# Optimization experiments

Measured on AMD Instinct MI355X. Metric: run time of the kernel, lower is better.

The kernel has to match this reference:

```python
import jax, jax.numpy as jnp
import numpy as np

TEMPERATURE = 0.1


def setup_inputs() -> dict:
    key = jax.random.key(0)
    k1, k2 = jax.random.split(key)
    B, D = 4096, 128
    z_i = jax.random.normal(k1, (B, D), dtype=jnp.float32)
    z_j = jax.random.normal(k2, (B, D), dtype=jnp.float32)
    return {"z_i": z_i, "z_j": z_j}


def reference(z_i, z_j):
    B = z_i.shape[0]
    n = 2 * B
    z = jnp.concatenate([z_i, z_j], axis=0)            # [2B, D]
    sim = jnp.matmul(z, z.T) / TEMPERATURE             # [2B, 2B]
    # positives: diag(sim, +B) and diag(sim, -B)
    pos = jnp.concatenate([jnp.diagonal(sim, B), jnp.diagonal(sim, -B)])[:, None]  # [2B, 1]
    # negatives: sim with diagonal removed, row-wise -> [2B, 2B-1]
    # strided trick equivalent to sim[~eye].reshape(n, n-1)
    neg = sim.ravel()[:-1].reshape(n - 1, n + 1)[:, 1:].reshape(n, n - 1)
    logits = jnp.concatenate([pos, neg], axis=1)       # [2B, 2B]
    # cross-entropy with labels all zero (positive in column 0)
    loss = jnp.mean(jax.nn.logsumexp(logits, axis=1) - logits[:, 0])
    return loss
```

## Files before the change

### kernel.cpp

```cpp
#include <hip/hip_runtime.h>
#include <stdint.h>

#define N_TOT  8192
#define BHALF  4096
#define DDIM   128
#define NSPLIT 32

typedef short bf16x8 __attribute__((ext_vector_type(8)));
typedef float f32x4  __attribute__((ext_vector_type(4)));

__device__ __forceinline__ float ex2(float x) { return __builtin_amdgcn_exp2f(x); }

__device__ __forceinline__ unsigned short f2bf(float f) {
    uint32_t u = __builtin_bit_cast(uint32_t, f);
    u += 0x7fff + ((u >> 16) & 1);
    return (unsigned short)(u >> 16);
}

__global__ void k_prep(const float* __restrict__ zi, const float* __restrict__ zj,
                       unsigned short* __restrict__ zb, float* __restrict__ pos) {
    const float c = 3.798282440185f;
    int i    = blockIdx.x * 4 + (threadIdx.x >> 6);
    int lane = threadIdx.x & 63;
    const float2 a = *reinterpret_cast<const float2*>(zi + i * DDIM + lane * 2);
    const float2 b = *reinterpret_cast<const float2*>(zj + i * DDIM + lane * 2);
    ushort2 oa, ob;
    oa.x = f2bf(a.x * c); oa.y = f2bf(a.y * c);
    ob.x = f2bf(b.x * c); ob.y = f2bf(b.y * c);
    *reinterpret_cast<ushort2*>(zb + i * DDIM + lane * 2) = oa;
    *reinterpret_cast<ushort2*>(zb + (i + BHALF) * DDIM + lane * 2) = ob;
    float p = a.x * b.x + a.y * b.y;
    #pragma unroll
    for (int m = 32; m; m >>= 1) p += __shfl_xor(p, m, 64);
    if (lane == 0) { pos[i] = 10.f * p; pos[i + BHALF] = 10.f * p; }
}

__launch_bounds__(512, 4)
__global__ void k_main(const unsigned short* __restrict__ zb,
                       float* __restrict__ pm, float* __restrict__ pl) {
    __shared__ unsigned short lds[64 * 128];
    const int tid  = threadIdx.x;
    const int w    = tid >> 6, lane = tid & 63;
    const int q    = lane >> 4, ln = lane & 15;
    const int rb   = blockIdx.x >> 5, cs = blockIdx.x & 31;
    const int rowBase = rb * 256 + w * 32;
    const int colBase = cs * 256;

    bf16x8 afr[2][4];
    #pragma unroll
    for (int s = 0; s < 2; ++s) {
        const unsigned short* p = zb + (rowBase + s * 16 + ln) * DDIM + q * 8;
        #pragma unroll
        for (int kc = 0; kc < 4; ++kc)
            afr[s][kc] = *reinterpret_cast<const bf16x8*>(p + kc * 32);
    }

    float m[2][4], l[2][4];
    #pragma unroll
    for (int s = 0; s < 2; ++s)
        #pragma unroll
        for (int r = 0; r < 4; ++r) { m[s][r] = -1e38f; l[s][r] = 0.f; }

    for (int ch = 0; ch < 4; ++ch) {
        #pragma unroll
        for (int it = 0; it < 2; ++it) {
            int idx  = it * 512 + tid;
            int col  = idx >> 4, g = idx & 15;
            int slot = g ^ (col & 7);
            const uint4* gp = reinterpret_cast<const uint4*>(
                zb + (colBase + ch * 64 + col) * DDIM + g * 8);
            *reinterpret_cast<uint4*>(&lds[col * 128 + slot * 8]) = *gp;
        }
        __syncthreads();

        #pragma unroll
        for (int ct = 0; ct < 4; ++ct) {
            bf16x8 bfr[4];
            #pragma unroll
            for (int kc = 0; kc < 4; ++kc) {
                int slot = (q + 4 * kc) ^ (ln & 7);
                bfr[kc] = *reinterpret_cast<const bf16x8*>(
                    &lds[(ct * 16 + ln) * 128 + slot * 8]);
            }
            const int colTile = colBase + ch * 64 + ct * 16;

            #pragma unroll
            for (int s = 0; s < 2; ++s) {
                f32x4 acc = {0.f, 0.f, 0.f, 0.f};
                #pragma unroll
                for (int kc = 0; kc < 4; ++kc)
                    acc = __builtin_amdgcn_mfma_f32_16x16x32_bf16(
                        afr[s][kc], bfr[kc], acc, 0, 0, 0);
                if (colTile == rowBase + s * 16) {
                    #pragma unroll
                    for (int r = 0; r < 4; ++r)
                        if (ln == q * 4 + r) acc[r] = -__builtin_inff();
                }
                #pragma unroll
                for (int r = 0; r < 4; ++r) {
                    float t  = acc[r];
                    float mo = m[s][r];
                    float mn = fmaxf(mo, t);
                    float pv = ex2(t - mn);
                    float sc = ex2(mo - mn);
                    l[s][r] = fmaf(l[s][r], sc, pv);
                    m[s][r] = mn;
                }
            }
        }
        __syncthreads();
    }

    #pragma unroll
    for (int s = 0; s < 2; ++s) {
        #pragma unroll
        for (int r = 0; r < 4; ++r) {
            float mm = m[s][r], ll = l[s][r];
            #pragma unroll
            for (int msk = 1; msk < 16; msk <<= 1) {
                float om = __shfl_xor(mm, msk, 64);
                float ol = __shfl_xor(ll, msk, 64);
                float mn = fmaxf(mm, om);
                ll = ll * ex2(mm - mn) + ol * ex2(om - mn);
                mm = mn;
            }
            if (ln == 0) {
                int row = rowBase + s * 16 + q * 4 + r;
                pm[cs * N_TOT + row] = mm;
                pl[cs * N_TOT + row] = ll;
            }
        }
    }
}

__global__ void k_finish(const float* __restrict__ pm, const float* __restrict__ pl,
                         const float* __restrict__ pos, float* __restrict__ partial) {
    int row = blockIdx.x * 256 + threadIdx.x;
    float p  = pos[row];
    float tp = p * 1.4426950408889634f;
    float mm[NSPLIT];
    float M = tp;
    #pragma unroll
    for (int j = 0; j < NSPLIT; ++j) {
        mm[j] = pm[j * N_TOT + row];
        M = fmaxf(M, mm[j]);
    }
    float S = ex2(tp - M);
    #pragma unroll
    for (int j = 0; j < NSPLIT; ++j)
        S += pl[j * N_TOT + row] * ex2(mm[j] - M);
    float lse = (M + __log2f(S)) * 0.6931471805599453f;
    float li  = lse - p;
    #pragma unroll
    for (int msk = 32; msk; msk >>= 1) li += __shfl_xor(li, msk, 64);
    __shared__ float red[4];
    if ((threadIdx.x & 63) == 0) red[threadIdx.x >> 6] = li;
    __syncthreads();
    if (threadIdx.x == 0)
        partial[blockIdx.x] = red[0] + red[1] + red[2] + red[3];
}

__global__ void k_sum(const float* __restrict__ partial, float* __restrict__ out) {
    int lane = threadIdx.x & 63;
    float v = (lane < 32) ? partial[lane] : 0.f;
    #pragma unroll
    for (int msk = 32; msk; msk >>= 1) v += __shfl_xor(v, msk, 64);
    if (lane == 0) out[0] = v * (1.f / 8192.f);
}

extern "C" void kernel_launch(void* const* d_in, const int* in_sizes, int n_in,
                              void* d_out, int out_size, void* d_ws, size_t ws_size,
                              hipStream_t stream) {
    const float* zi = (const float*)d_in[0];
    const float* zj = (const float*)d_in[1];
    float* out = (float*)d_out;
    char* ws = (char*)d_ws;

    unsigned short* zb = (unsigned short*)ws;
    float* pos         = (float*)(ws + (size_t)2 * 1024 * 1024);
    float* pm          = pos + N_TOT;
    float* pl          = pm + NSPLIT * N_TOT;
    float* partial     = pl + NSPLIT * N_TOT;

    hipLaunchKernelGGL(k_prep,   dim3(1024), dim3(256), 0, stream, zi, zj, zb, pos);
    hipLaunchKernelGGL(k_main,   dim3(1024), dim3(512), 0, stream, zb, pm, pl);
    hipLaunchKernelGGL(k_finish, dim3(32),   dim3(256), 0, stream, pm, pl, pos, partial);
    hipLaunchKernelGGL(k_sum,    dim3(1),    dim3(64),  0, stream, partial, out);
}
```

Baseline: 100.9 us.

## Fuse bf16 conversion into main kernel, double-buffer LDS, drop prep and sum kernels

Removes the separate prep kernel by loading fp32 inputs directly in the main kernel and converting them to bf16 on the fly. Column tiles are now double-buffered in LDS with register prefetch. Each block covers twice as many columns (16 splits instead of 32), and the online softmax update handles two column tiles per step. The positive-pair dot product moves into the finish kernel, which accumulates the mean with an atomicAdd, so the final sum kernel and two launches are gone. In exchange every block converts fp32 to bf16 redundantly, reads twice as many input bytes, and doubles its LDS use, and the atomic sum makes float accumulation order nondeterministic.

```diff
diff --git a/kernel.cpp b/kernel.cpp
--- a/kernel.cpp
+++ b/kernel.cpp
@@ -1,58 +1,89 @@
 #include <hip/hip_runtime.h>
+#include <hip/hip_bf16.h>
 #include <stdint.h>
 
 #define N_TOT  8192
 #define BHALF  4096
 #define DDIM   128
-#define NSPLIT 32
+#define NSPLIT 16
 
 typedef short bf16x8 __attribute__((ext_vector_type(8)));
 typedef float f32x4  __attribute__((ext_vector_type(4)));
 
 __device__ __forceinline__ float ex2(float x) { return __builtin_amdgcn_exp2f(x); }
 
-__device__ __forceinline__ unsigned short f2bf(float f) {
-    uint32_t u = __builtin_bit_cast(uint32_t, f);
-    u += 0x7fff + ((u >> 16) & 1);
-    return (unsigned short)(u >> 16);
-}
-
-__global__ void k_prep(const float* __restrict__ zi, const float* __restrict__ zj,
-                       unsigned short* __restrict__ zb, float* __restrict__ pos) {
-    const float c = 3.798282440185f;
-    int i    = blockIdx.x * 4 + (threadIdx.x >> 6);
-    int lane = threadIdx.x & 63;
-    const float2 a = *reinterpret_cast<const float2*>(zi + i * DDIM + lane * 2);
-    const float2 b = *reinterpret_cast<const float2*>(zj + i * DDIM + lane * 2);
-    ushort2 oa, ob;
-    oa.x = f2bf(a.x * c); oa.y = f2bf(a.y * c);
-    ob.x = f2bf(b.x * c); ob.y = f2bf(b.y * c);
-    *reinterpret_cast<ushort2*>(zb + i * DDIM + lane * 2) = oa;
-    *reinterpret_cast<ushort2*>(zb + (i + BHALF) * DDIM + lane * 2) = ob;
-    float p = a.x * b.x + a.y * b.y;
-    #pragma unroll
-    for (int m = 32; m; m >>= 1) p += __shfl_xor(p, m, 64);
-    if (lane == 0) { pos[i] = 10.f * p; pos[i + BHALF] = 10.f * p; }
+#define SCALE_C 3.798282440185f
+
+__device__ __forceinline__ ushort2 cvt2(float a, float b) {
+    __hip_bfloat162 h = __float22bfloat162_rn(make_float2(a, b));
+    return *reinterpret_cast<ushort2*>(&h);
+}
+
+__device__ __forceinline__ bf16x8 cvt8(float4 lo, float4 hi) {
+    union { bf16x8 v; ushort2 u[4]; } r;
+    r.u[0] = cvt2(lo.x * SCALE_C, lo.y * SCALE_C);
+    r.u[1] = cvt2(lo.z * SCALE_C, lo.w * SCALE_C);
+    r.u[2] = cvt2(hi.x * SCALE_C, hi.y * SCALE_C);
+    r.u[3] = cvt2(hi.z * SCALE_C, hi.w * SCALE_C);
+    return r.v;
+}
+
+struct StageRegs { float4 v[4]; };
+
+__device__ __forceinline__ StageRegs stage_load(const float* __restrict__ zi,
+                                                const float* __restrict__ zj,
+                                                int colBase, int ch, int tid) {
+    StageRegs s;
+    #pragma unroll
+    for (int it = 0; it < 2; ++it) {
+        int idx  = it * 512 + tid;
+        int col  = idx >> 4, g = idx & 15;
+        int gcol = colBase + ch * 64 + col;
+        const float* cp = (gcol < BHALF) ? zi + gcol * DDIM
+                                         : zj + (gcol - BHALF) * DDIM;
+        s.v[it * 2]     = *reinterpret_cast<const float4*>(cp + g * 8);
+        s.v[it * 2 + 1] = *reinterpret_cast<const float4*>(cp + g * 8 + 4);
+    }
+    return s;
+}
+
+__device__ __forceinline__ void stage_write(const StageRegs& s, int tid,
+                                            unsigned short* buf) {
+    #pragma unroll
+    for (int it = 0; it < 2; ++it) {
+        int idx  = it * 512 + tid;
+        int col  = idx >> 4, g = idx & 15;
+        int slot = g ^ (col & 7);
+        *reinterpret_cast<bf16x8*>(&buf[col * 128 + slot * 8]) =
+            cvt8(s.v[it * 2], s.v[it * 2 + 1]);
+    }
 }
 
 __launch_bounds__(512, 4)
-__global__ void k_main(const unsigned short* __restrict__ zb,
-                       float* __restrict__ pm, float* __restrict__ pl) {
-    __shared__ unsigned short lds[64 * 128];
-    const int tid  = threadIdx.x;
-    const int w    = tid >> 6, lane = tid & 63;
-    const int q    = lane >> 4, ln = lane & 15;
-    const int rb   = blockIdx.x >> 5, cs = blockIdx.x & 31;
+__global__ void k_main(const float* __restrict__ zi, const float* __restrict__ zj,
+                       float* __restrict__ pm, float* __restrict__ pl,
+                       float* __restrict__ out) {
+    if (blockIdx.x == 0 && threadIdx.x == 0) out[0] = 0.f;
+    __shared__ unsigned short lds[2][64 * 128];
+    const int tid = threadIdx.x;
+    const int w = tid >> 6, lane = tid & 63;
+    const int q = lane >> 4, ln = lane & 15;
+    const int rb = blockIdx.x >> 4, cs = blockIdx.x & 15;
     const int rowBase = rb * 256 + w * 32;
-    const int colBase = cs * 256;
+    const int colBase = cs * 512;
 
     bf16x8 afr[2][4];
     #pragma unroll
     for (int s = 0; s < 2; ++s) {
-        const unsigned short* p = zb + (rowBase + s * 16 + ln) * DDIM + q * 8;
-        #pragma unroll
-        for (int kc = 0; kc < 4; ++kc)
-            afr[s][kc] = *reinterpret_cast<const bf16x8*>(p + kc * 32);
+        int row = rowBase + s * 16 + ln;
+        const float* rp = (row < BHALF) ? zi + row * DDIM
+                                        : zj + (row - BHALF) * DDIM;
+        #pragma unroll
+        for (int kc = 0; kc < 4; ++kc) {
+            float4 lo = *reinterpret_cast<const float4*>(rp + kc * 32 + q * 8);
+            float4 hi = *reinterpret_cast<const float4*>(rp + kc * 32 + q * 8 + 4);
+            afr[s][kc] = cvt8(lo, hi);
+        }
     }
 
     float m[2][4], l[2][4];
@@ -61,53 +92,67 @@
         #pragma unroll
         for (int r = 0; r < 4; ++r) { m[s][r] = -1e38f; l[s][r] = 0.f; }
 
-    for (int ch = 0; ch < 4; ++ch) {
-        #pragma unroll
-        for (int it = 0; it < 2; ++it) {
-            int idx  = it * 512 + tid;
-            int col  = idx >> 4, g = idx & 15;
-            int slot = g ^ (col & 7);
-            const uint4* gp = reinterpret_cast<const uint4*>(
-                zb + (colBase + ch * 64 + col) * DDIM + g * 8);
-            *reinterpret_cast<uint4*>(&lds[col * 128 + slot * 8]) = *gp;
-        }
-        __syncthreads();
-
-        #pragma unroll
-        for (int ct = 0; ct < 4; ++ct) {
-            bf16x8 bfr[4];
-            #pragma unroll
-            for (int kc = 0; kc < 4; ++kc) {
-                int slot = (q + 4 * kc) ^ (ln & 7);
-                bfr[kc] = *reinterpret_cast<const bf16x8*>(
-                    &lds[(ct * 16 + ln) * 128 + slot * 8]);
-            }
-            const int colTile = colBase + ch * 64 + ct * 16;
-
+    StageRegs sr = stage_load(zi, zj, colBase, 0, tid);
+    stage_write(sr, tid, lds[0]);
+    __syncthreads();
+
+    for (int ch = 0; ch < 8; ++ch) {
+        const unsigned short* buf = lds[ch & 1];
+        if (ch < 7) sr = stage_load(zi, zj, colBase, ch + 1, tid);
+
+        #pragma unroll
+        for (int ct2 = 0; ct2 < 2; ++ct2) {
+            f32x4 acc[2][2];
+            #pragma unroll
+            for (int s = 0; s < 2; ++s)
+                #pragma unroll
+                for (int u = 0; u < 2; ++u) acc[s][u] = (f32x4){0.f, 0.f, 0.f, 0.f};
+
+            #pragma unroll
+            for (int u = 0; u < 2; ++u) {
+                int ct = ct2 * 2 + u;
+                bf16x8 bfr[4];
+                #pragma unroll
+                for (int kc = 0; kc < 4; ++kc) {
+                    int slot = (q + 4 * kc) ^ (ln & 7);
+                    bfr[kc] = *reinterpret_cast<const bf16x8*>(
+                        &buf[(ct * 16 + ln) * 128 + slot * 8]);
+                }
+                #pragma unroll
+                for (int s = 0; s < 2; ++s)
+                    #pragma unroll
+                    for (int kc = 0; kc < 4; ++kc)
+                        acc[s][u] = __builtin_amdgcn_mfma_f32_16x16x32_bf16(
+                            afr[s][kc], bfr[kc], acc[s][u], 0, 0, 0);
+            }
+
+            const int c0 = colBase + ch * 64 + ct2 * 32;
             #pragma unroll
             for (int s = 0; s < 2; ++s) {
-                f32x4 acc = {0.f, 0.f, 0.f, 0.f};
-                #pragma unroll
-                for (int kc = 0; kc < 4; ++kc)
-                    acc = __builtin_amdgcn_mfma_f32_16x16x32_bf16(
-                        afr[s][kc], bfr[kc], acc, 0, 0, 0);
-                if (colTile == rowBase + s * 16) {
+                const int rt = rowBase + s * 16;
+                if (c0 == rt) {
                     #pragma unroll
                     for (int r = 0; r < 4; ++r)
-                        if (ln == q * 4 + r) acc[r] = -__builtin_inff();
+                        if (ln == q * 4 + r) acc[s][0][r] = -__builtin_inff();
+                } else if (c0 + 16 == rt) {
+                    #pragma unroll
+                    for (int r = 0; r < 4; ++r)
+                        if (ln == q * 4 + r) acc[s][1][r] = -__builtin_inff();
                 }
                 #pragma unroll
                 for (int r = 0; r < 4; ++r) {
-                    float t  = acc[r];
+                    float t0 = acc[s][0][r], t1 = acc[s][1][r];
                     float mo = m[s][r];
-                    float mn = fmaxf(mo, t);
-                    float pv = ex2(t - mn);
+                    float mn = fmaxf(fmaxf(t0, t1), mo);
                     float sc = ex2(mo - mn);
+                    float pv = ex2(t0 - mn) + ex2(t1 - mn);
                     l[s][r] = fmaf(l[s][r], sc, pv);
                     m[s][r] = mn;
                 }
             }
         }
+
+        if (ch < 7) stage_write(sr, tid, lds[(ch + 1) & 1]);
         __syncthreads();
     }
 
@@ -133,10 +178,20 @@
     }
 }
 
-__global__ void k_finish(const float* __restrict__ pm, const float* __restrict__ pl,
-                         const float* __restrict__ pos, float* __restrict__ partial) {
+__global__ void k_finish(const float* __restrict__ zi, const float* __restrict__ zj,
+                         const float* __restrict__ pm, const float* __restrict__ pl,
+                         float* __restrict__ out) {
     int row = blockIdx.x * 256 + threadIdx.x;
-    float p  = pos[row];
+    int pr  = row & (BHALF - 1);
+    const float4* a = reinterpret_cast<const float4*>(zi + pr * DDIM);
+    const float4* b = reinterpret_cast<const float4*>(zj + pr * DDIM);
+    float acc = 0.f;
+    #pragma unroll
+    for (int k = 0; k < 32; ++k) {
+        float4 x = a[k], y = b[k];
+        acc += x.x * y.x + x.y * y.y + x.z * y.z + x.w * y.w;
+    }
+    float p  = 10.f * acc;
     float tp = p * 1.4426950408889634f;
     float mm[NSPLIT];
     float M = tp;
@@ -157,15 +212,7 @@
     if ((threadIdx.x & 63) == 0) red[threadIdx.x >> 6] = li;
     __syncthreads();
     if (threadIdx.x == 0)
-        partial[blockIdx.x] = red[0] + red[1] + red[2] + red[3];
-}
-
-__global__ void k_sum(const float* __restrict__ partial, float* __restrict__ out) {
-    int lane = threadIdx.x & 63;
-    float v = (lane < 32) ? partial[lane] : 0.f;
-    #pragma unroll
-    for (int msk = 32; msk; msk >>= 1) v += __shfl_xor(v, msk, 64);
-    if (lane == 0) out[0] = v * (1.f / 8192.f);
+        atomicAdd(out, (red[0] + red[1] + red[2] + red[3]) * (1.f / 8192.f));
 }
 
 extern "C" void kernel_launch(void* const* d_in, const int* in_sizes, int n_in,
@@ -176,14 +223,9 @@
     float* out = (float*)d_out;
     char* ws = (char*)d_ws;
 
-    unsigned short* zb = (unsigned short*)ws;
-    float* pos         = (float*)(ws + (size_t)2 * 1024 * 1024);
-    float* pm          = pos + N_TOT;
-    float* pl          = pm + NSPLIT * N_TOT;
-    float* partial     = pl + NSPLIT * N_TOT;
-
-    hipLaunchKernelGGL(k_prep,   dim3(1024), dim3(256), 0, stream, zi, zj, zb, pos);
-    hipLaunchKernelGGL(k_main,   dim3(1024), dim3(512), 0, stream, zb, pm, pl);
-    hipLaunchKernelGGL(k_finish, dim3(32),   dim3(256), 0, stream, pm, pl, pos, partial);
-    hipLaunchKernelGGL(k_sum,    dim3(1),    dim3(64),  0, stream, partial, out);
-}
+    float* pm = (float*)ws;
+    float* pl = pm + NSPLIT * N_TOT;
+
+    hipLaunchKernelGGL(k_main,   dim3(512), dim3(512), 0, stream, zi, zj, pm, pl, out);
+    hipLaunchKernelGGL(k_finish, dim3(32),  dim3(256), 0, stream, zi, zj, pm, pl, out);
+}
```

Result: no change. 99.93 us (-1.0%).
